# Optimization experiments

Hardware: AMD Instinct MI355X
Metric: run time of the kernel (lower is better)

The kernel has to match this reference:

```python
import jax, jax.numpy as jnp
from jax import lax
import numpy as np

BS, NQ, NC, T = 64, 300, 2, 16  # batch, queries, classes, targets per video
COST_CLASS = 1.0
COST_BBOX = 1.0
COST_GIOU = 1.0
FG_LABEL = 0
BIG = jnp.float32(1e9)


def setup_inputs() -> dict:
    key = jax.random.key(0)
    k1, k2, k3 = jax.random.split(key, 3)
    return {
        'pred_logits': jax.random.normal(k1, (BS, NQ, NC), jnp.float32),
        'pred_boxes': jax.random.uniform(k2, (BS, NQ, 4), jnp.float32),
        'tgt_bbox': jax.random.uniform(k3, (BS * T, 4), jnp.float32),
    }


def box_cxcywh_to_xyxy(b):
    cx, cy, w, h = b[..., 0], b[..., 1], b[..., 2], b[..., 3]
    return jnp.stack([cx - 0.5 * w, cy - 0.5 * h, cx + 0.5 * w, cy + 0.5 * h], axis=-1)


def generalized_box_iou(b1, b2):
    # b1: [N,4], b2: [M,4] in xyxy -> [N,M] GIoU
    area1 = (b1[:, 2] - b1[:, 0]) * (b1[:, 3] - b1[:, 1])
    area2 = (b2[:, 2] - b2[:, 0]) * (b2[:, 3] - b2[:, 1])
    lt = jnp.maximum(b1[:, None, :2], b2[None, :, :2])
    rb = jnp.minimum(b1[:, None, 2:], b2[None, :, 2:])
    wh = jnp.clip(rb - lt, 0.0)
    inter = wh[..., 0] * wh[..., 1]
    union = area1[:, None] + area2[None, :] - inter
    iou = inter / union
    lte = jnp.minimum(b1[:, None, :2], b2[None, :, :2])
    rbe = jnp.maximum(b1[:, None, 2:], b2[None, :, 2:])
    whe = jnp.clip(rbe - lte, 0.0)
    areae = whe[..., 0] * whe[..., 1]
    return iou - (areae - union) / areae


def cost_matrix(pred_logits, pred_boxes, tgt_bbox):
    out_prob = jax.nn.softmax(pred_logits.reshape(-1, pred_logits.shape[-1]), axis=-1)  # [BS*NQ, NC]
    out_bbox = pred_boxes.reshape(-1, 4)  # [BS*NQ, 4]
    # tgt_ids are all the foreground label -> gather column FG_LABEL, broadcast over targets
    cost_class = -out_prob[:, FG_LABEL][:, None]  # [BS*NQ, 1]
    cost_bbox = jnp.abs(out_bbox[:, None, :] - tgt_bbox[None, :, :]).sum(-1)  # L1 cdist [N, M]
    cost_giou = -generalized_box_iou(box_cxcywh_to_xyxy(out_bbox), box_cxcywh_to_xyxy(tgt_bbox))
    C = COST_BBOX * cost_bbox + COST_GIOU * cost_giou + COST_CLASS * cost_class
    return C.reshape(pred_logits.shape[0], pred_logits.shape[1], -1)  # [BS, NQ, BS*T]


def hungarian(cost_tq):
    # Exact Jonker-Volgenant / e-maxx Hungarian. cost_tq: [n, m] with n <= m
    # (rows = targets, cols = queries). Returns (row_ind, col_ind) matching
    # scipy.optimize.linear_sum_assignment on the [m, n] (query x target) matrix.
    n, m = cost_tq.shape
    ca = jnp.zeros((n + 1, m + 1), cost_tq.dtype).at[1:, 1:].set(cost_tq)

    def outer(i, uvp):
        u, v, p = uvp
        p = p.at[0].set(i.astype(jnp.int32))
        minv = jnp.full(m + 1, BIG, ca.dtype)
        used = jnp.zeros(m + 1, bool)
        way = jnp.zeros(m + 1, jnp.int32)
        j0 = jnp.int32(0)

        def cond(st):
            u, v, p, minv, used, way, j0 = st
            return p[j0] != 0

        def body(st):
            u, v, p, minv, used, way, j0 = st
            used = used.at[j0].set(True)
            i0 = p[j0]
            cur = ca[i0] - u[i0] - v  # reduced costs of row i0 vs all columns
            upd = (~used) & (cur < minv)
            minv = jnp.where(upd, cur, minv)
            way = jnp.where(upd, j0, way)
            masked = jnp.where(used, BIG, minv)
            j1 = jnp.argmin(masked).astype(jnp.int32)
            delta = masked[j1]
            add = jnp.where(used, delta, 0.0)
            u = u.at[p].add(add)  # u[p[j]] += delta for used j (index 0 is dummy)
            v = v - add
            minv = jnp.where(used, minv, minv - delta)
            return (u, v, p, minv, used, way, j1)

        u, v, p, minv, used, way, j0 = lax.while_loop(cond, body, (u, v, p, minv, used, way, j0))

        def acond(st):
            j0, p = st
            return j0 != 0

        def abody(st):
            j0, p = st
            j1 = way[j0]
            p = p.at[j0].set(p[j1])
            return (j1, p)

        j0, p = lax.while_loop(acond, abody, (j0, p))
        return (u, v, p)

    u = jnp.zeros(n + 1, ca.dtype)
    v = jnp.zeros(m + 1, ca.dtype)
    p = jnp.zeros(m + 1, jnp.int32)
    u, v, p = lax.fori_loop(1, n + 1, outer, (u, v, p))
    assigned = p[1:]  # per query column: 1+target row, 0 if unassigned
    qidx = jnp.arange(m, dtype=jnp.int32)
    row_ind = jnp.sort(jnp.where(assigned > 0, qidx, m))[:n]  # sorted query indices
    col_ind = assigned[row_ind] - 1  # matched target indices
    return row_ind, col_ind


def reference(pred_logits, pred_boxes, tgt_bbox):
    bs, nq = pred_logits.shape[:2]
    t = tgt_bbox.shape[0] // bs  # uniform targets per video (static)
    C = cost_matrix(pred_logits, pred_boxes, tgt_bbox)  # [bs, nq, bs*t]
    # split(sizes, -1) with uniform sizes + per-batch diagonal block selection
    blocks = C.reshape(bs, nq, bs, t)
    Cb = blocks[jnp.arange(bs), :, jnp.arange(bs), :]  # [bs, nq, t]
    row_ind, col_ind = jax.vmap(hungarian)(jnp.swapaxes(Cb, 1, 2))  # solver wants [t, nq]
    return C, row_ind, col_ind
```

## Files before the change

### kernel.cpp

```cpp
#include <hip/hip_runtime.h>

#define BS 64
#define NQ 300
#define NTGT 1024
#define TT 16
#define MCOL 300
#define NROW 16
#define STR 304
#define BIGF 1000000000.0f

__device__ __forceinline__ float cell_cost(float p0, float pcx, float pcy, float pw, float ph,
                                           float px1, float py1, float px2, float py2, float parea,
                                           float4 tb)
{
    float cb = fabsf(pcx - tb.x) + fabsf(pcy - tb.y) + fabsf(pw - tb.z) + fabsf(ph - tb.w);
    float tx1 = tb.x - 0.5f*tb.z, ty1 = tb.y - 0.5f*tb.w;
    float tx2 = tb.x + 0.5f*tb.z, ty2 = tb.y + 0.5f*tb.w;
    float tarea = (tx2 - tx1) * (ty2 - ty1);
    float ltx = fmaxf(px1, tx1), lty = fmaxf(py1, ty1);
    float rbx = fminf(px2, tx2), rby = fminf(py2, ty2);
    float iw = fmaxf(rbx - ltx, 0.f), ih = fmaxf(rby - lty, 0.f);
    float inter = iw * ih;
    float uni = parea + tarea - inter;
    float iou = inter * __builtin_amdgcn_rcpf(uni);
    float ex1 = fminf(px1, tx1), ey1 = fminf(py1, ty1);
    float ex2 = fmaxf(px2, tx2), ey2 = fmaxf(py2, ty2);
    float areae = (ex2 - ex1) * (ey2 - ey1);
    float giou = iou - (areae - uni) * __builtin_amdgcn_rcpf(areae);
    return cb - giou - p0;
}

template<int CTRL>
__device__ __forceinline__ float dppmin_f(float x) {
    int t = __builtin_amdgcn_update_dpp(__float_as_int(BIGF), __float_as_int(x),
                                        CTRL, 0xF, 0xF, false);
    return fminf(x, __int_as_float(t));
}
template<int CTRL>
__device__ __forceinline__ int dppmin_i(int x) {
    int t = __builtin_amdgcn_update_dpp(0x7FFFFFFF, x, CTRL, 0xF, 0xF, false);
    return (t < x) ? t : x;
}
__device__ __forceinline__ float wave_min_f(float x) {
    x = dppmin_f<0x111>(x);
    x = dppmin_f<0x112>(x);
    x = dppmin_f<0x114>(x);
    x = dppmin_f<0x118>(x);
    x = dppmin_f<0x142>(x);
    x = dppmin_f<0x143>(x);
    return x;
}
__device__ __forceinline__ int wave_min_i(int x) {
    x = dppmin_i<0x111>(x);
    x = dppmin_i<0x112>(x);
    x = dppmin_i<0x114>(x);
    x = dppmin_i<0x118>(x);
    x = dppmin_i<0x142>(x);
    x = dppmin_i<0x143>(x);
    return x;
}

__device__ __forceinline__ int rl5(const int a[5], int k0, int l0) {
    int r0 = __builtin_amdgcn_readlane(a[0], l0);
    int r1 = __builtin_amdgcn_readlane(a[1], l0);
    int r2 = __builtin_amdgcn_readlane(a[2], l0);
    int r3 = __builtin_amdgcn_readlane(a[3], l0);
    int r4 = __builtin_amdgcn_readlane(a[4], l0);
    int r = r0;
    r = (k0 == 1) ? r1 : r;
    r = (k0 == 2) ? r2 : r;
    r = (k0 == 3) ? r3 : r;
    r = (k0 == 4) ? r4 : r;
    return r;
}
__device__ __forceinline__ float rl5f(const float a[5], int k0, int l0) {
    int ai[5] = { __float_as_int(a[0]), __float_as_int(a[1]), __float_as_int(a[2]),
                  __float_as_int(a[3]), __float_as_int(a[4]) };
    return __int_as_float(rl5(ai, k0, l0));
}

__global__ __launch_bounds__(256) void fused_kernel(
    const float* __restrict__ logits,
    const float* __restrict__ boxes,
    const float* __restrict__ tgt,
    float* __restrict__ out)
{
    __shared__ float ca[16 * STR + 32];
    const int tid = threadIdx.x;

    if (blockIdx.x >= BS) {
        int q = blockIdx.x - BS;
        float l0v = logits[2*q], l1v = logits[2*q + 1];
        float p0 = __builtin_amdgcn_rcpf(1.f + __expf(l1v - l0v));
        float4 pb = ((const float4*)boxes)[q];
        float px1 = pb.x - 0.5f*pb.z, py1 = pb.y - 0.5f*pb.w;
        float px2 = pb.x + 0.5f*pb.z, py2 = pb.y + 0.5f*pb.w;
        float parea = (px2 - px1) * (py2 - py1);

        int t0 = tid << 2;
        const float4* tgt4 = (const float4*)tgt;
        float4 tb0 = tgt4[t0+0], tb1 = tgt4[t0+1], tb2 = tgt4[t0+2], tb3 = tgt4[t0+3];
        float4 r;
        r.x = cell_cost(p0, pb.x, pb.y, pb.z, pb.w, px1, py1, px2, py2, parea, tb0);
        r.y = cell_cost(p0, pb.x, pb.y, pb.z, pb.w, px1, py1, px2, py2, parea, tb1);
        r.z = cell_cost(p0, pb.x, pb.y, pb.z, pb.w, px1, py1, px2, py2, parea, tb2);
        r.w = cell_cost(p0, pb.x, pb.y, pb.z, pb.w, px1, py1, px2, py2, parea, tb3);
        *(float4*)(out + (size_t)q * NTGT + t0) = r;
        return;
    }

    const int b = blockIdx.x;

    {
        auto fill_row = [&](int q) {
            float l0v = logits[(b*NQ + q)*2 + 0], l1v = logits[(b*NQ + q)*2 + 1];
            float p0 = __builtin_amdgcn_rcpf(1.f + __expf(l1v - l0v));
            float4 pb = ((const float4*)boxes)[b*NQ + q];
            float px1 = pb.x - 0.5f*pb.z, py1 = pb.y - 0.5f*pb.w;
            float px2 = pb.x + 0.5f*pb.z, py2 = pb.y + 0.5f*pb.w;
            float parea = (px2 - px1) * (py2 - py1);
            #pragma unroll
            for (int t = 0; t < TT; ++t) {
                float4 tb = ((const float4*)tgt)[b*TT + t];
                ca[t*STR + 1 + q] =
                    cell_cost(p0, pb.x, pb.y, pb.z, pb.w, px1, py1, px2, py2, parea, tb);
            }
        };
        fill_row(tid);
        if (tid >= 212) fill_row(tid + 44);
        if (tid < 16) ca[tid*STR] = 0.f;
    }
    __syncthreads();
    if (tid >= 64) return;

    __builtin_amdgcn_s_setprio(1);

    const int lane = tid;
    int   p_reg[5]   = {0,0,0,0,0};
    int   way_reg[5] = {0,0,0,0,0};
    float vloc[5]    = {0.f,0.f,0.f,0.f,0.f};
    float minv[5], ur_reg[5];
    float u_lane = 0.f;

    for (int i = 1; i <= NROW; ++i) {
        if (lane == 0) p_reg[0] = i;
        unsigned usedm = 0, treemask = 0;
        #pragma unroll
        for (int k = 0; k < 5; ++k) { minv[k] = BIGF; way_reg[k] = 0; }
        #pragma unroll
        for (int k = 0; k < 5; ++k) ur_reg[k] = __shfl(u_lane, p_reg[k], 64);

        int j0 = 0;
        for (;;) {
            int l0 = j0 & 63, k0 = j0 >> 6;
            int i0 = rl5(p_reg, k0, l0);
            if (i0 == 0) break;
            float ui0 = rl5f(ur_reg, k0, l0);
            if (lane == l0) usedm |= (1u << k0);
            treemask |= (1u << i0);

            int rowbase = (i0 - 1) * STR + lane;
            float cur[5];
            #pragma unroll
            for (int k = 0; k < 5; ++k) cur[k] = ca[rowbase + (k << 6)];

            float bestv = BIGF; int bestj = 0x7FFFFFFF;
            #pragma unroll
            for (int k = 0; k < 5; ++k) {
                int j = lane + (k << 6);
                bool act = (j <= MCOL);
                bool us  = ((usedm >> k) & 1u) != 0u;
                float cu = cur[k] - ui0 - vloc[k];
                if (act && !us && cu < minv[k]) { minv[k] = cu; way_reg[k] = j0; }
                float mk = (act && !us) ? minv[k] : BIGF;
                if (mk < bestv) { bestv = mk; bestj = j; }
            }
            float mv = wave_min_f(bestv);
            float delta = __int_as_float(
                __builtin_amdgcn_readlane(__float_as_int(mv), 63));
            int cand = (bestv == delta) ? bestj : 0x7FFFFFFF;
            int cm = wave_min_i(cand);
            int j1 = __builtin_amdgcn_readlane(cm, 63);

            #pragma unroll
            for (int k = 0; k < 5; ++k) {
                bool us = ((usedm >> k) & 1u) != 0u;
                if (us) { vloc[k] -= delta; ur_reg[k] += delta; }
                else if (lane + (k << 6) <= MCOL) minv[k] -= delta;
            }
            if (lane <= NROW && ((treemask >> lane) & 1u)) u_lane += delta;
            j0 = j1;
        }
        while (j0 != 0) {
            int l0 = j0 & 63, k0 = j0 >> 6;
            int jn = rl5(way_reg, k0, l0);
            int pn = rl5(p_reg, jn >> 6, jn & 63);
            #pragma unroll
            for (int k = 0; k < 5; ++k)
                if (k == k0 && lane == l0) p_reg[k] = pn;
            j0 = jn;
        }
    }

    __builtin_amdgcn_s_setprio(0);

    const size_t ROWB = (size_t)BS * NQ * NTGT;
    const size_t COLB = ROWB + (size_t)BS * TT;
    int base = 0;
    #pragma unroll
    for (int k = 0; k < 5; ++k) {
        int pk1 = (k < 4) ? __shfl(p_reg[k + 1], 0, 64) : 0;
        int psh = __shfl(p_reg[k], (lane + 1) & 63, 64);
        int q = (k << 6) | lane;
        int a = (lane == 63) ? pk1 : psh;
        if (q >= MCOL) a = 0;
        unsigned long long mb = __ballot(a > 0);
        int pos = base + __popcll(mb & ((1ull << lane) - 1ull));
        if (a > 0) {
            out[ROWB + (size_t)b * TT + pos] = (float)q;
            out[COLB + (size_t)b * TT + pos] = (float)(a - 1);
        }
        base += __popcll(mb);
    }
}

extern "C" void kernel_launch(void* const* d_in, const int* in_sizes, int n_in,
                              void* d_out, int out_size, void* d_ws, size_t ws_size,
                              hipStream_t stream) {
    const float* logits = (const float*)d_in[0];
    const float* boxes  = (const float*)d_in[1];
    const float* tgt    = (const float*)d_in[2];
    float* out = (float*)d_out;

    fused_kernel<<<dim3(BS + BS*NQ), 256, 0, stream>>>(logits, boxes, tgt, out);
}
```

Before: 31.31 us.

## Cache cost rows in registers and streamline Hungarian inner loop selection

Loads the full 16x300 per-batch cost block into 80 registers per lane up front, so the Hungarian inner loop reads rows through a switch instead of LDS loads. Used columns are excluded by subtracting a large bias from the working potential rather than by per-iteration masks, and the per-lane argmin becomes a branchless tree. When exactly one lane holds the minimum, the second wave reduction is replaced by a ballot plus readlane, and readlane calls are cut from five to one through a select-then-readlane pattern. The risks are high register pressure or spills from the 80-entry array, and a divergent switch on a uniform index that may compile to a jump table.

Result: slower. 39.91 us (+27.5%).

```diff
diff --git a/kernel.cpp b/kernel.cpp
--- a/kernel.cpp
+++ b/kernel.cpp
@@ -8,6 +8,8 @@
 #define NROW 16
 #define STR 304
 #define BIGF 1000000000.0f
+#define BIG2 2000000000.0f
+#define BIG4 4000000000.0f
 
 __device__ __forceinline__ float cell_cost(float p0, float pcx, float pcy, float pw, float ph,
                                            float px1, float py1, float px2, float py2, float parea,
@@ -60,23 +62,21 @@
     return x;
 }
 
-__device__ __forceinline__ int rl5(const int a[5], int k0, int l0) {
-    int r0 = __builtin_amdgcn_readlane(a[0], l0);
-    int r1 = __builtin_amdgcn_readlane(a[1], l0);
-    int r2 = __builtin_amdgcn_readlane(a[2], l0);
-    int r3 = __builtin_amdgcn_readlane(a[3], l0);
-    int r4 = __builtin_amdgcn_readlane(a[4], l0);
-    int r = r0;
-    r = (k0 == 1) ? r1 : r;
-    r = (k0 == 2) ? r2 : r;
-    r = (k0 == 3) ? r3 : r;
-    r = (k0 == 4) ? r4 : r;
+__device__ __forceinline__ int sel5i(const int a[5], int k0) {
+    int r = a[0];
+    r = (k0 == 1) ? a[1] : r;
+    r = (k0 == 2) ? a[2] : r;
+    r = (k0 == 3) ? a[3] : r;
+    r = (k0 == 4) ? a[4] : r;
     return r;
 }
-__device__ __forceinline__ float rl5f(const float a[5], int k0, int l0) {
-    int ai[5] = { __float_as_int(a[0]), __float_as_int(a[1]), __float_as_int(a[2]),
-                  __float_as_int(a[3]), __float_as_int(a[4]) };
-    return __int_as_float(rl5(ai, k0, l0));
+__device__ __forceinline__ float sel5f(const float a[5], int k0) {
+    float r = a[0];
+    r = (k0 == 1) ? a[1] : r;
+    r = (k0 == 2) ? a[2] : r;
+    r = (k0 == 3) ? a[3] : r;
+    r = (k0 == 4) ? a[4] : r;
+    return r;
 }
 
 __global__ __launch_bounds__(256) void fused_kernel(
@@ -136,65 +136,96 @@
     __builtin_amdgcn_s_setprio(1);
 
     const int lane = tid;
+
+    float R[16][5];
+    #pragma unroll
+    for (int t = 0; t < 16; ++t) {
+        #pragma unroll
+        for (int k = 0; k < 4; ++k)
+            R[t][k] = ca[t*STR + lane + (k << 6)];
+        R[t][4] = (lane <= 44) ? ca[t*STR + lane + 256] : BIG4;
+    }
+
     int   p_reg[5]   = {0,0,0,0,0};
     int   way_reg[5] = {0,0,0,0,0};
     float vloc[5]    = {0.f,0.f,0.f,0.f,0.f};
-    float minv[5], ur_reg[5];
+    float w[5], minv[5], ur_reg[5];
     float u_lane = 0.f;
 
     for (int i = 1; i <= NROW; ++i) {
         if (lane == 0) p_reg[0] = i;
         unsigned usedm = 0, treemask = 0;
         #pragma unroll
-        for (int k = 0; k < 5; ++k) { minv[k] = BIGF; way_reg[k] = 0; }
+        for (int k = 0; k < 5; ++k) { minv[k] = BIGF; way_reg[k] = 0; w[k] = vloc[k]; }
         #pragma unroll
         for (int k = 0; k < 5; ++k) ur_reg[k] = __shfl(u_lane, p_reg[k], 64);
 
         int j0 = 0;
         for (;;) {
             int l0 = j0 & 63, k0 = j0 >> 6;
-            int i0 = rl5(p_reg, k0, l0);
+            int i0 = __builtin_amdgcn_readlane(sel5i(p_reg, k0), l0);
             if (i0 == 0) break;
-            float ui0 = rl5f(ur_reg, k0, l0);
-            if (lane == l0) usedm |= (1u << k0);
+            float ui0 = __int_as_float(
+                __builtin_amdgcn_readlane(__float_as_int(sel5f(ur_reg, k0)), l0));
+            #pragma unroll
+            for (int k = 0; k < 5; ++k)
+                if (k == k0 && lane == l0) { usedm |= (1u << k); w[k] -= BIG2; minv[k] = BIGF; }
             treemask |= (1u << i0);
 
-            int rowbase = (i0 - 1) * STR + lane;
-            float cur[5];
-            #pragma unroll
-            for (int k = 0; k < 5; ++k) cur[k] = ca[rowbase + (k << 6)];
-
-            float bestv = BIGF; int bestj = 0x7FFFFFFF;
+            float c0, c1, c2, c3, c4;
+            switch (i0) {
+#define ROWCASE(T) case (T)+1: c0=R[T][0]; c1=R[T][1]; c2=R[T][2]; c3=R[T][3]; c4=R[T][4]; break;
+                ROWCASE(0)  ROWCASE(1)  ROWCASE(2)  ROWCASE(3)
+                ROWCASE(4)  ROWCASE(5)  ROWCASE(6)  ROWCASE(7)
+                ROWCASE(8)  ROWCASE(9)  ROWCASE(10) ROWCASE(11)
+                ROWCASE(12) ROWCASE(13) ROWCASE(14) ROWCASE(15)
+#undef ROWCASE
+                default: __builtin_unreachable();
+            }
+
+            float cu[5];
+            cu[0] = c0 - ui0 - w[0];
+            cu[1] = c1 - ui0 - w[1];
+            cu[2] = c2 - ui0 - w[2];
+            cu[3] = c3 - ui0 - w[3];
+            cu[4] = c4 - ui0 - w[4];
             #pragma unroll
             for (int k = 0; k < 5; ++k) {
-                int j = lane + (k << 6);
-                bool act = (j <= MCOL);
-                bool us  = ((usedm >> k) & 1u) != 0u;
-                float cu = cur[k] - ui0 - vloc[k];
-                if (act && !us && cu < minv[k]) { minv[k] = cu; way_reg[k] = j0; }
-                float mk = (act && !us) ? minv[k] : BIGF;
-                if (mk < bestv) { bestv = mk; bestj = j; }
-            }
-            float mv = wave_min_f(bestv);
-            float delta = __int_as_float(
-                __builtin_amdgcn_readlane(__float_as_int(mv), 63));
-            int cand = (bestv == delta) ? bestj : 0x7FFFFFFF;
-            int cm = wave_min_i(cand);
-            int j1 = __builtin_amdgcn_readlane(cm, 63);
+                bool lt = cu[k] < minv[k];
+                way_reg[k] = lt ? j0 : way_reg[k];
+                minv[k] = lt ? cu[k] : minv[k];
+            }
+            float v01 = fminf(minv[0], minv[1]); int j01 = (minv[0] <= minv[1]) ? lane : lane + 64;
+            float v23 = fminf(minv[2], minv[3]); int j23 = (minv[2] <= minv[3]) ? lane + 128 : lane + 192;
+            float v03 = fminf(v01, v23);         int j03 = (v01 <= v23) ? j01 : j23;
+            float bv  = fminf(v03, minv[4]);     int bj  = (v03 <= minv[4]) ? j03 : lane + 256;
+
+            float mv = wave_min_f(bv);
+            float delta = __int_as_float(__builtin_amdgcn_readlane(__float_as_int(mv), 63));
+            unsigned long long eq = __ballot(bv == delta);
+            int j1;
+            if (__popcll(eq) == 1) {
+                j1 = __builtin_amdgcn_readlane(bj, (int)(__ffsll((unsigned long long)eq) - 1));
+            } else {
+                int cand = (bv == delta) ? bj : 0x7FFFFFFF;
+                j1 = __builtin_amdgcn_readlane(wave_min_i(cand), 63);
+            }
 
             #pragma unroll
             for (int k = 0; k < 5; ++k) {
                 bool us = ((usedm >> k) & 1u) != 0u;
-                if (us) { vloc[k] -= delta; ur_reg[k] += delta; }
-                else if (lane + (k << 6) <= MCOL) minv[k] -= delta;
+                vloc[k]   = us ? vloc[k] - delta   : vloc[k];
+                w[k]      = us ? w[k] - delta      : w[k];
+                ur_reg[k] = us ? ur_reg[k] + delta : ur_reg[k];
+                minv[k]   = us ? minv[k]           : minv[k] - delta;
             }
             if (lane <= NROW && ((treemask >> lane) & 1u)) u_lane += delta;
             j0 = j1;
         }
         while (j0 != 0) {
             int l0 = j0 & 63, k0 = j0 >> 6;
-            int jn = rl5(way_reg, k0, l0);
-            int pn = rl5(p_reg, jn >> 6, jn & 63);
+            int jn = __builtin_amdgcn_readlane(sel5i(way_reg, k0), l0);
+            int pn = __builtin_amdgcn_readlane(sel5i(p_reg, jn >> 6), jn & 63);
             #pragma unroll
             for (int k = 0; k < 5; ++k)
                 if (k == k0 && lane == l0) p_reg[k] = pn;
```

## Warm-start Hungarian duals with row minima and simplify lane register reads

Applied to the files above, without the earlier changes.

Before the assignment loop, the row potentials u are set to each target row's minimum cost. This is a row-reduction warm start intended to shorten the Dijkstra-style augmenting searches. The per-column copy of u (ur_reg) is dropped, and u is read directly from the owning lane by one readlane. The 5-way readlane-then-select helper becomes a register select followed by a single readlane, cutting scalar read instructions on the serial critical path. The warm start adds 16 wave reductions up front and could change which assignment is chosen among equal-cost ties.

New measurement: 39.99 us. +27.7%, slower.

```diff
diff --git a/kernel.cpp b/kernel.cpp
--- a/kernel.cpp
+++ b/kernel.cpp
@@ -60,23 +60,13 @@
     return x;
 }
 
-__device__ __forceinline__ int rl5(const int a[5], int k0, int l0) {
-    int r0 = __builtin_amdgcn_readlane(a[0], l0);
-    int r1 = __builtin_amdgcn_readlane(a[1], l0);
-    int r2 = __builtin_amdgcn_readlane(a[2], l0);
-    int r3 = __builtin_amdgcn_readlane(a[3], l0);
-    int r4 = __builtin_amdgcn_readlane(a[4], l0);
-    int r = r0;
-    r = (k0 == 1) ? r1 : r;
-    r = (k0 == 2) ? r2 : r;
-    r = (k0 == 3) ? r3 : r;
-    r = (k0 == 4) ? r4 : r;
+__device__ __forceinline__ int sel5i(const int a[5], int k0) {
+    int r = a[0];
+    r = (k0 == 1) ? a[1] : r;
+    r = (k0 == 2) ? a[2] : r;
+    r = (k0 == 3) ? a[3] : r;
+    r = (k0 == 4) ? a[4] : r;
     return r;
-}
-__device__ __forceinline__ float rl5f(const float a[5], int k0, int l0) {
-    int ai[5] = { __float_as_int(a[0]), __float_as_int(a[1]), __float_as_int(a[2]),
-                  __float_as_int(a[3]), __float_as_int(a[4]) };
-    return __int_as_float(rl5(ai, k0, l0));
 }
 
 __global__ __launch_bounds__(256) void fused_kernel(
@@ -136,26 +126,41 @@
     __builtin_amdgcn_s_setprio(1);
 
     const int lane = tid;
+
+    float u_lane = 0.f;
+    #pragma unroll
+    for (int t = 0; t < 16; ++t) {
+        float loc = BIGF;
+        #pragma unroll
+        for (int k = 0; k < 5; ++k) {
+            int j = lane + (k << 6);
+            float c = ca[t*STR + j];
+            bool ok = (j >= 1) && (j <= MCOL);
+            loc = fminf(loc, ok ? c : BIGF);
+        }
+        float rm = __int_as_float(
+            __builtin_amdgcn_readlane(__float_as_int(wave_min_f(loc)), 63));
+        if (lane == t + 1) u_lane = rm;
+    }
+
     int   p_reg[5]   = {0,0,0,0,0};
     int   way_reg[5] = {0,0,0,0,0};
     float vloc[5]    = {0.f,0.f,0.f,0.f,0.f};
-    float minv[5], ur_reg[5];
-    float u_lane = 0.f;
+    float minv[5];
 
     for (int i = 1; i <= NROW; ++i) {
         if (lane == 0) p_reg[0] = i;
         unsigned usedm = 0, treemask = 0;
         #pragma unroll
         for (int k = 0; k < 5; ++k) { minv[k] = BIGF; way_reg[k] = 0; }
-        #pragma unroll
-        for (int k = 0; k < 5; ++k) ur_reg[k] = __shfl(u_lane, p_reg[k], 64);
 
         int j0 = 0;
         for (;;) {
             int l0 = j0 & 63, k0 = j0 >> 6;
-            int i0 = rl5(p_reg, k0, l0);
+            int i0 = __builtin_amdgcn_readlane(sel5i(p_reg, k0), l0);
             if (i0 == 0) break;
-            float ui0 = rl5f(ur_reg, k0, l0);
+            float ui0 = __int_as_float(
+                __builtin_amdgcn_readlane(__float_as_int(u_lane), i0));
             if (lane == l0) usedm |= (1u << k0);
             treemask |= (1u << i0);
 
@@ -176,8 +181,7 @@
                 if (mk < bestv) { bestv = mk; bestj = j; }
             }
             float mv = wave_min_f(bestv);
-            float delta = __int_as_float(
-                __builtin_amdgcn_readlane(__float_as_int(mv), 63));
+            float delta = __int_as_float(__builtin_amdgcn_readlane(__float_as_int(mv), 63));
             int cand = (bestv == delta) ? bestj : 0x7FFFFFFF;
             int cm = wave_min_i(cand);
             int j1 = __builtin_amdgcn_readlane(cm, 63);
@@ -185,7 +189,7 @@
             #pragma unroll
             for (int k = 0; k < 5; ++k) {
                 bool us = ((usedm >> k) & 1u) != 0u;
-                if (us) { vloc[k] -= delta; ur_reg[k] += delta; }
+                if (us) { vloc[k] -= delta; }
                 else if (lane + (k << 6) <= MCOL) minv[k] -= delta;
             }
             if (lane <= NROW && ((treemask >> lane) & 1u)) u_lane += delta;
@@ -193,8 +197,8 @@
         }
         while (j0 != 0) {
             int l0 = j0 & 63, k0 = j0 >> 6;
-            int jn = rl5(way_reg, k0, l0);
-            int pn = rl5(p_reg, jn >> 6, jn & 63);
+            int jn = __builtin_amdgcn_readlane(sel5i(way_reg, k0), l0);
+            int pn = __builtin_amdgcn_readlane(sel5i(p_reg, jn >> 6), jn & 63);
             #pragma unroll
             for (int k = 0; k < 5; ++k)
                 if (k == k0 && lane == l0) p_reg[k] = pn;
```
